# Kernel optimization log

Measured on AMD Instinct MI355X. Metric: run time of the kernel, lower is better.

## Reference

```python
import jax, jax.numpy as jnp
import numpy as np

B, S, D, H = 2, 2048, 512, 8
DK = D // H
MASK_VALUE = -1e9


def setup_inputs() -> dict:
    key = jax.random.key(0)
    ks = jax.random.split(key, 12)
    scale = 1.0 / np.sqrt(D)
    inp = {
        "query": jax.random.normal(ks[0], (B, S, D), jnp.float32),
        "key": jax.random.normal(ks[1], (B, S, D), jnp.float32),
        "value": jax.random.normal(ks[2], (B, S, D), jnp.float32),
        # causal mask, broadcastable over batch and heads
        "mask": jnp.tril(jnp.ones((S, S), jnp.int32))[None, None, :, :],
        "Wq": jax.random.normal(ks[3], (D, D), jnp.float32) * scale,
        "bq": jax.random.normal(ks[4], (D,), jnp.float32) * scale,
        "Wk": jax.random.normal(ks[5], (D, D), jnp.float32) * scale,
        "bk": jax.random.normal(ks[6], (D,), jnp.float32) * scale,
        "Wv": jax.random.normal(ks[7], (D, D), jnp.float32) * scale,
        "bv": jax.random.normal(ks[8], (D,), jnp.float32) * scale,
        "Wo": jax.random.normal(ks[9], (D, D), jnp.float32) * scale,
        "bo": jax.random.normal(ks[10], (D,), jnp.float32) * scale,
    }
    return inp


def reference(query, key, value, mask, Wq, bq, Wk, bk, Wv, bv, Wo, bo):
    # linear projections (torch Linear: x @ W.T + b)
    q = query @ Wq.T + bq
    k = key @ Wk.T + bk
    v = value @ Wv.T + bv
    # split heads: [B,S,D] -> [B,H,S,DK]
    q = q.reshape(B, S, H, DK).transpose(0, 2, 1, 3)
    k = k.reshape(B, S, H, DK).transpose(0, 2, 1, 3)
    v = v.reshape(B, S, H, DK).transpose(0, 2, 1, 3)
    # scaled dot-product attention with explicit [B,H,S,S] score matrix
    scores = jnp.einsum("bhqd,bhkd->bhqk", q, k) / jnp.sqrt(jnp.float32(DK))
    scores = jnp.where(mask == 0, jnp.float32(MASK_VALUE), scores)
    attn = jax.nn.softmax(scores, axis=-1)
    x = jnp.einsum("bhqk,bhkd->bhqd", attn, v)
    # merge heads: [B,H,S,DK] -> [B,S,D]
    x = x.transpose(0, 2, 1, 3).reshape(B, S, D)
    return x @ Wo.T + bo
```

## Files before the change

kernel.cpp:

```cpp
#include <hip/hip_runtime.h>
#include <hip/hip_bf16.h>

#define B_   2
#define S_   2048
#define D_   512
#define H_   8
#define DK_  64
#define M_   (B_*S_)

typedef float  floatx4 __attribute__((ext_vector_type(4)));
typedef __bf16 bf16x8  __attribute__((ext_vector_type(8)));

#define MFMA16x16x32(a,b,c) __builtin_amdgcn_mfma_f32_16x16x32_bf16((a),(b),(c),0,0,0)

static __device__ __forceinline__ void load_lds16(const void* g, void* l) {
  __builtin_amdgcn_global_load_lds(
      (const __attribute__((address_space(1))) void*)g,
      (__attribute__((address_space(3))) void*)l,
      16, 0, 0);
}

__global__ __launch_bounds__(256) void cvt_inputs(
    const float* __restrict__ w0, const float* __restrict__ w1,
    const float* __restrict__ w2, const float* __restrict__ w3,
    const float* __restrict__ x0, const float* __restrict__ x1,
    const float* __restrict__ x2,
    __bf16* __restrict__ out)
{
  const int idx = (blockIdx.x * 256 + threadIdx.x) * 4;
  const float* src;
  int off;
  if (idx < 1048576) {
    src = (idx < 524288) ? ((idx < 262144) ? w0 : w1)
                         : ((idx < 786432) ? w2 : w3);
    off = idx & 0x3FFFF;
  } else {
    const int i2 = idx - 1048576;
    const int xs = i2 >> 21;
    src = (xs == 0) ? x0 : (xs == 1) ? x1 : x2;
    off = i2 & 0x1FFFFF;
  }
  float4 v = *(const float4*)(src + off);
  __bf16* o = out + idx;
  o[0]=(__bf16)v.x; o[1]=(__bf16)v.y; o[2]=(__bf16)v.z; o[3]=(__bf16)v.w;
}


__global__ __launch_bounds__(256) void proj_qkv(
    const __bf16* __restrict__ Xb, const __bf16* __restrict__ Wball,
    const float* __restrict__ bq, const float* __restrict__ bk, const float* __restrict__ bv,
    __bf16* __restrict__ Qb, __bf16* __restrict__ Kb, __bf16* __restrict__ Vtb)
{
  __shared__ __align__(16) __bf16 abuf[2][128*32];
  __shared__ __align__(16) __bf16 bbuf[2][128*32];

  const int z = blockIdx.z;
  const __bf16* X    = Xb + (size_t)z * (M_*D_);
  const __bf16* W    = Wball + (size_t)z * (D_*D_);
  const float*  bias = (z==0) ? bq : (z==1) ? bk : bv;

  const int m0 = blockIdx.x * 128;
  const int n0 = blockIdx.y * 128;
  const int tid  = threadIdx.x;
  const int w    = tid >> 6;
  const int lane = tid & 63;
  const int lcol = lane & 15;
  const int quad = lane >> 4;
  const int wm = w >> 1, wn = w & 1;

  floatx4 zero = {0.f,0.f,0.f,0.f};
  floatx4 acc[4][4];
#pragma unroll
  for (int i = 0; i < 4; ++i)
#pragma unroll
    for (int nt = 0; nt < 4; ++nt) acc[i][nt] = zero;

  auto stage = [&](int bsel, int k0) {
#pragma unroll
    for (int j = 0; j < 2; ++j) {
      const int u0 = (j*4 + w) * 64;
      const int u  = u0 + lane;
      const int row = u >> 2, c16 = (u & 3) * 8;
      load_lds16(X + (size_t)(m0 + row)*D_ + k0 + c16,
                 (char*)&abuf[bsel][0] + u0*16);
      load_lds16(W + (size_t)(n0 + row)*D_ + k0 + c16,
                 (char*)&bbuf[bsel][0] + u0*16);
    }
  };

  stage(0, 0);
  for (int it = 0; it < 16; ++it) {
    __syncthreads();
    if (it + 1 < 16) stage((it+1)&1, (it+1)*32);
    const __bf16* ab = &abuf[it&1][0];
    const __bf16* bb = &bbuf[it&1][0];
    bf16x8 af[4], bf[4];
#pragma unroll
    for (int i = 0; i < 4; ++i)
      af[i] = *(const bf16x8*)(ab + (wm*64 + i*16 + lcol)*32 + quad*8);
#pragma unroll
    for (int nt = 0; nt < 4; ++nt)
      bf[nt] = *(const bf16x8*)(bb + (wn*64 + nt*16 + lcol)*32 + quad*8);
#pragma unroll
    for (int i = 0; i < 4; ++i)
#pragma unroll
      for (int nt = 0; nt < 4; ++nt)
        acc[i][nt] = MFMA16x16x32(af[i], bf[nt], acc[i][nt]);
  }

#pragma unroll
  for (int nt = 0; nt < 4; ++nt) {
    const int n = n0 + wn*64 + nt*16 + lcol;
    const float bias_n = bias[n];
    const int hh = n >> 6, dk = n & 63;
#pragma unroll
    for (int i = 0; i < 4; ++i)
#pragma unroll
      for (int r = 0; r < 4; ++r) {
        const int m  = m0 + wm*64 + i*16 + quad*4 + r;
        const int bb2 = m >> 11, ss = m & (S_-1);
        const float val = acc[i][nt][r] + bias_n;
        if (z == 0) {
          Qb[(((size_t)(bb2*H_+hh))*S_ + ss)*DK_ + dk] = (__bf16)val;
        } else if (z == 1) {
          const int cch = ss >> 6, klo = ss & 63;
          const int knt = klo >> 4, klc = klo & 15;
          const int ks = dk >> 5, qd = (dk >> 3) & 3, jj = dk & 7;
          Kb[((size_t)(bb2*H_+hh))*S_*DK_ + (size_t)cch*4096 +
             (((knt*2+ks)*64 + qd*16 + klc)*8 + jj)] = (__bf16)val;
        } else {
          const int cch = ss >> 6, klo = ss & 63;
          const int ks = klo >> 5, qd = (klo >> 3) & 3, jj = klo & 7;
          const int vnt = dk >> 4, vlc = dk & 15;
          Vtb[((size_t)(bb2*H_+hh))*DK_*S_ + (size_t)cch*4096 +
              (((vnt*2+ks)*64 + qd*16 + vlc)*8 + jj)] = (__bf16)val;
        }
      }
  }
}

__global__ __launch_bounds__(256) void attn_fwd(
    const __bf16* __restrict__ Qb, const __bf16* __restrict__ Kb,
    const __bf16* __restrict__ Vtb, __bf16* __restrict__ attnb)
{
  __shared__ __align__(16) __bf16 kbuf[2][64*64];
  __shared__ __align__(16) __bf16 vbuf[2][64*64];
  __shared__ __align__(16) __bf16 pbuf[4][16*72];

  const int tid  = threadIdx.x;
  const int w    = tid >> 6;
  const int lane = tid & 63;
  const int lcol = lane & 15;
  const int quad = lane >> 4;
  const int hh = blockIdx.y;
  const int bb = blockIdx.z;

  const int t   = 31 - blockIdx.x;
  const int q0  = t * 64;
  const int qr0 = q0 + w*16;

  const __bf16* Qp = Qb  + (size_t)(bb*H_ + hh) * S_ * DK_;
  const __bf16* Kp = Kb  + (size_t)(bb*H_ + hh) * S_ * DK_;
  const __bf16* Vp = Vtb + (size_t)(bb*H_ + hh) * DK_ * S_;

  const bf16x8 aq0 = *(const bf16x8*)(Qp + (size_t)(qr0 + lcol)*DK_ + quad*8);
  const bf16x8 aq1 = *(const bf16x8*)(Qp + (size_t)(qr0 + lcol)*DK_ + 32 + quad*8);

  floatx4 zero = {0.f,0.f,0.f,0.f};
  floatx4 acc[4] = {zero, zero, zero, zero};
  float lsum[4] = {0.f, 0.f, 0.f, 0.f};

  auto stage_chunk = [&](int bsel, int c) {
    const char* ksrc = (const char*)(Kp + (size_t)c * 4096);
    const char* vsrc = (const char*)(Vp + (size_t)c * 4096);
#pragma unroll
    for (int j = 0; j < 2; ++j) {
      const int off = w*2048 + j*1024;
      load_lds16(ksrc + off + lane*16, (char*)kbuf[bsel] + off);
      load_lds16(vsrc + off + lane*16, (char*)vbuf[bsel] + off);
    }
  };

  const int nch = t + 1;
  stage_chunk(0, 0);
  for (int c = 0; c < nch; ++c) {
    __syncthreads();
    if (c + 1 < nch) stage_chunk((c+1)&1, c+1);
    const int bsel = c & 1;
    const int k0 = c * 64;
    const __bf16* kb = kbuf[bsel];
    const __bf16* vb = vbuf[bsel];

    floatx4 s[4];
#pragma unroll
    for (int nt = 0; nt < 4; ++nt) {
      bf16x8 kf0 = *(const bf16x8*)(kb + (nt*2+0)*512 + lane*8);
      bf16x8 kf1 = *(const bf16x8*)(kb + (nt*2+1)*512 + lane*8);
      s[nt] = MFMA16x16x32(aq1, kf1, MFMA16x16x32(aq0, kf0, zero));
    }

    const bool edge = (k0 + 63 > qr0);
#pragma unroll
    for (int nt = 0; nt < 4; ++nt) {
#pragma unroll
      for (int r = 0; r < 4; ++r) {
        float p = __expf(s[nt][r] * 0.125f);
        if (edge) {
          const int qrow = qr0 + quad*4 + r;
          if (k0 + nt*16 + lcol > qrow) p = 0.f;
        }
        lsum[r] += p;
        pbuf[w][(quad*4 + r)*72 + nt*16 + lcol] = (__bf16)p;
      }
    }
    asm volatile("s_waitcnt lgkmcnt(0)" ::: "memory");

    const bf16x8 pa0 = *(const bf16x8*)(&pbuf[w][lcol*72 + quad*8]);
    const bf16x8 pa1 = *(const bf16x8*)(&pbuf[w][lcol*72 + 32 + quad*8]);
#pragma unroll
    for (int nt = 0; nt < 4; ++nt) {
      bf16x8 vf0 = *(const bf16x8*)(vb + (nt*2+0)*512 + lane*8);
      bf16x8 vf1 = *(const bf16x8*)(vb + (nt*2+1)*512 + lane*8);
      acc[nt] = MFMA16x16x32(pa0, vf0, acc[nt]);
      acc[nt] = MFMA16x16x32(pa1, vf1, acc[nt]);
    }
  }

  float rinv[4];
#pragma unroll
  for (int r = 0; r < 4; ++r) {
    float tv = lsum[r];
    tv += __shfl_xor(tv, 1, 16);
    tv += __shfl_xor(tv, 2, 16);
    tv += __shfl_xor(tv, 4, 16);
    tv += __shfl_xor(tv, 8, 16);
    rinv[r] = 1.0f / tv;
  }

#pragma unroll
  for (int nt = 0; nt < 4; ++nt)
#pragma unroll
    for (int r = 0; r < 4; ++r) {
      const int q = qr0 + quad*4 + r;
      attnb[((size_t)(bb*S_ + q)) * D_ + hh*DK_ + nt*16 + lcol] =
          (__bf16)(acc[nt][r] * rinv[r]);
    }
}

__global__ __launch_bounds__(256) void proj_out(
    const __bf16* __restrict__ attnb, const __bf16* __restrict__ Wob,
    const float* __restrict__ bo, float* __restrict__ out)
{
  __shared__ __align__(16) __bf16 abuf[2][128*32];
  __shared__ __align__(16) __bf16 bbuf[2][128*32];

  const int m0 = blockIdx.x * 128;
  const int n0 = blockIdx.y * 128;
  const int tid  = threadIdx.x;
  const int w    = tid >> 6;
  const int lane = tid & 63;
  const int lcol = lane & 15;
  const int quad = lane >> 4;
  const int wm = w >> 1, wn = w & 1;

  floatx4 zero = {0.f,0.f,0.f,0.f};
  floatx4 acc[4][4];
#pragma unroll
  for (int i = 0; i < 4; ++i)
#pragma unroll
    for (int nt = 0; nt < 4; ++nt) acc[i][nt] = zero;

  auto stage = [&](int bsel, int k0) {
#pragma unroll
    for (int j = 0; j < 2; ++j) {
      const int u0 = (j*4 + w) * 64;
      const int u  = u0 + lane;
      const int row = u >> 2, c16 = (u & 3) * 8;
      load_lds16(attnb + (size_t)(m0 + row)*D_ + k0 + c16,
                 (char*)&abuf[bsel][0] + u0*16);
      load_lds16(Wob + (size_t)(n0 + row)*D_ + k0 + c16,
                 (char*)&bbuf[bsel][0] + u0*16);
    }
  };

  stage(0, 0);
  for (int it = 0; it < 16; ++it) {
    __syncthreads();
    if (it + 1 < 16) stage((it+1)&1, (it+1)*32);
    const __bf16* ab = &abuf[it&1][0];
    const __bf16* bb = &bbuf[it&1][0];
    bf16x8 af[4], bf[4];
#pragma unroll
    for (int i = 0; i < 4; ++i)
      af[i] = *(const bf16x8*)(ab + (wm*64 + i*16 + lcol)*32 + quad*8);
#pragma unroll
    for (int nt = 0; nt < 4; ++nt)
      bf[nt] = *(const bf16x8*)(bb + (wn*64 + nt*16 + lcol)*32 + quad*8);
#pragma unroll
    for (int i = 0; i < 4; ++i)
#pragma unroll
      for (int nt = 0; nt < 4; ++nt)
        acc[i][nt] = MFMA16x16x32(af[i], bf[nt], acc[i][nt]);
  }

#pragma unroll
  for (int nt = 0; nt < 4; ++nt) {
    const int n = n0 + wn*64 + nt*16 + lcol;
    const float bias_n = bo[n];
#pragma unroll
    for (int i = 0; i < 4; ++i)
#pragma unroll
      for (int r = 0; r < 4; ++r) {
        const int m = m0 + wm*64 + i*16 + quad*4 + r;
        out[(size_t)m * D_ + n] = acc[i][nt][r] + bias_n;
      }
  }
}

extern "C" void kernel_launch(void* const* d_in, const int* in_sizes, int n_in,
                              void* d_out, int out_size, void* d_ws, size_t ws_size,
                              hipStream_t stream) {
  const float* q_in = (const float*)d_in[0];
  const float* k_in = (const float*)d_in[1];
  const float* v_in = (const float*)d_in[2];
  const float* Wq = (const float*)d_in[4];
  const float* bq = (const float*)d_in[5];
  const float* Wk = (const float*)d_in[6];
  const float* bk = (const float*)d_in[7];
  const float* Wv = (const float*)d_in[8];
  const float* bv = (const float*)d_in[9];
  const float* Wo = (const float*)d_in[10];
  const float* bo = (const float*)d_in[11];
  float* out = (float*)d_out;

  __bf16* ws    = (__bf16*)d_ws;
  __bf16* Qb    = ws;
  __bf16* Kb    = ws + 1*2097152;
  __bf16* Vtb   = ws + 2*2097152;
  __bf16* attnb = ws + 3*2097152;
  __bf16* Wb    = ws + 4*2097152;
  __bf16* Xb    = Wb + 4*262144;

  cvt_inputs<<<dim3(7168), dim3(256), 0, stream>>>(
      Wq, Wk, Wv, Wo, q_in, k_in, v_in, Wb);

  proj_qkv<<<dim3(M_/128, D_/128, 3), dim3(256), 0, stream>>>(
      Xb, Wb, bq, bk, bv, Qb, Kb, Vtb);

  attn_fwd<<<dim3(32, H_, B_), dim3(256), 0, stream>>>(Qb, Kb, Vtb, attnb);

  proj_out<<<dim3(M_/128, D_/128), dim3(256), 0, stream>>>(
      attnb, Wb + 3*262144, bo, out);
}
```

Measured before the change: 177.7 us.

## Stage QKV projection outputs through LDS and halve attention query tile

The QKV projection epilogue now writes its results into shared memory in the target per-head layouts (Q row-major, K and V pre-swizzled) and then copies them out with coalesced 16-byte stores, replacing scattered 2-byte global writes. The attention kernel moves from 64-row query tiles with 4 waves to 32-row tiles with 2 waves, doubling the grid to spread the causal workload across more blocks. In exchange, each attention block now reloads K/V chunks for fewer query rows, adding global and LDS traffic.

```diff
diff --git a/kernel.cpp b/kernel.cpp
--- a/kernel.cpp
+++ b/kernel.cpp
@@ -51,8 +51,7 @@
     const float* __restrict__ bq, const float* __restrict__ bk, const float* __restrict__ bv,
     __bf16* __restrict__ Qb, __bf16* __restrict__ Kb, __bf16* __restrict__ Vtb)
 {
-  __shared__ __align__(16) __bf16 abuf[2][128*32];
-  __shared__ __align__(16) __bf16 bbuf[2][128*32];
+  __shared__ __align__(16) __bf16 smem[16384];
 
   const int z = blockIdx.z;
   const __bf16* X    = Xb + (size_t)z * (M_*D_);
@@ -82,9 +81,9 @@
       const int u  = u0 + lane;
       const int row = u >> 2, c16 = (u & 3) * 8;
       load_lds16(X + (size_t)(m0 + row)*D_ + k0 + c16,
-                 (char*)&abuf[bsel][0] + u0*16);
+                 (char*)(smem + bsel*4096) + u0*16);
       load_lds16(W + (size_t)(n0 + row)*D_ + k0 + c16,
-                 (char*)&bbuf[bsel][0] + u0*16);
+                 (char*)(smem + 8192 + bsel*4096) + u0*16);
     }
   };
 
@@ -92,8 +91,8 @@
   for (int it = 0; it < 16; ++it) {
     __syncthreads();
     if (it + 1 < 16) stage((it+1)&1, (it+1)*32);
-    const __bf16* ab = &abuf[it&1][0];
-    const __bf16* bb = &bbuf[it&1][0];
+    const __bf16* ab = smem + (it&1)*4096;
+    const __bf16* bb = smem + 8192 + (it&1)*4096;
     bf16x8 af[4], bf[4];
 #pragma unroll
     for (int i = 0; i < 4; ++i)
@@ -108,44 +107,55 @@
         acc[i][nt] = MFMA16x16x32(af[i], bf[nt], acc[i][nt]);
   }
 
+  __syncthreads();
 #pragma unroll
   for (int nt = 0; nt < 4; ++nt) {
     const int n = n0 + wn*64 + nt*16 + lcol;
     const float bias_n = bias[n];
-    const int hh = n >> 6, dk = n & 63;
+    const int h_l = (n >> 6) & 1;
+    const int dk  = n & 63;
 #pragma unroll
     for (int i = 0; i < 4; ++i)
 #pragma unroll
       for (int r = 0; r < 4; ++r) {
-        const int m  = m0 + wm*64 + i*16 + quad*4 + r;
-        const int bb2 = m >> 11, ss = m & (S_-1);
+        const int m = m0 + wm*64 + i*16 + quad*4 + r;
         const float val = acc[i][nt][r] + bias_n;
+        const int p = h_l*2 + ((m >> 6) & 1);
+        const int klo = m & 63;
+        int off;
         if (z == 0) {
-          Qb[(((size_t)(bb2*H_+hh))*S_ + ss)*DK_ + dk] = (__bf16)val;
+          off = klo*64 + dk;
         } else if (z == 1) {
-          const int cch = ss >> 6, klo = ss & 63;
-          const int knt = klo >> 4, klc = klo & 15;
-          const int ks = dk >> 5, qd = (dk >> 3) & 3, jj = dk & 7;
-          Kb[((size_t)(bb2*H_+hh))*S_*DK_ + (size_t)cch*4096 +
-             (((knt*2+ks)*64 + qd*16 + klc)*8 + jj)] = (__bf16)val;
+          off = (((klo>>4)*2 + (dk>>5))*64 + ((dk>>3)&3)*16 + (klo&15))*8 + (dk&7);
         } else {
-          const int cch = ss >> 6, klo = ss & 63;
-          const int ks = klo >> 5, qd = (klo >> 3) & 3, jj = klo & 7;
-          const int vnt = dk >> 4, vlc = dk & 15;
-          Vtb[((size_t)(bb2*H_+hh))*DK_*S_ + (size_t)cch*4096 +
-              (((vnt*2+ks)*64 + qd*16 + vlc)*8 + jj)] = (__bf16)val;
+          off = (((dk>>4)*2 + (klo>>5))*64 + ((klo>>3)&3)*16 + (dk&15))*8 + (klo&7);
         }
+        smem[p*4096 + off] = (__bf16)val;
       }
   }
-}
-
-__global__ __launch_bounds__(256) void attn_fwd(
+  __syncthreads();
+
+  __bf16* dst = (z==0) ? Qb : (z==1) ? Kb : Vtb;
+  const int bb2  = m0 >> 11;
+  const int hh0  = n0 >> 6;
+  const int cc0  = (m0 & 2047) >> 6;
+#pragma unroll
+  for (int it2 = 0; it2 < 8; ++it2) {
+    const int u = it2*256 + tid;
+    const int p = u >> 9, o = u & 511;
+    const size_t base = ((size_t)(bb2*H_ + hh0 + (p>>1)))*(S_*DK_)
+                      + (size_t)(cc0 + (p&1))*4096;
+    *(bf16x8*)(dst + base + o*8) = *(const bf16x8*)(smem + p*4096 + o*8);
+  }
+}
+
+__global__ __launch_bounds__(128) void attn_fwd(
     const __bf16* __restrict__ Qb, const __bf16* __restrict__ Kb,
     const __bf16* __restrict__ Vtb, __bf16* __restrict__ attnb)
 {
-  __shared__ __align__(16) __bf16 kbuf[2][64*64];
-  __shared__ __align__(16) __bf16 vbuf[2][64*64];
-  __shared__ __align__(16) __bf16 pbuf[4][16*72];
+  __shared__ __align__(16) __bf16 kbuf[2][4096];
+  __shared__ __align__(16) __bf16 vbuf[2][4096];
+  __shared__ __align__(16) __bf16 pbuf[2][16*72];
 
   const int tid  = threadIdx.x;
   const int w    = tid >> 6;
@@ -155,8 +165,8 @@
   const int hh = blockIdx.y;
   const int bb = blockIdx.z;
 
-  const int t   = 31 - blockIdx.x;
-  const int q0  = t * 64;
+  const int t   = 63 - blockIdx.x;
+  const int q0  = t * 32;
   const int qr0 = q0 + w*16;
 
   const __bf16* Qp = Qb  + (size_t)(bb*H_ + hh) * S_ * DK_;
@@ -174,14 +184,14 @@
     const char* ksrc = (const char*)(Kp + (size_t)c * 4096);
     const char* vsrc = (const char*)(Vp + (size_t)c * 4096);
 #pragma unroll
-    for (int j = 0; j < 2; ++j) {
-      const int off = w*2048 + j*1024;
+    for (int j = 0; j < 4; ++j) {
+      const int off = (j*2 + w) * 1024;
       load_lds16(ksrc + off + lane*16, (char*)kbuf[bsel] + off);
       load_lds16(vsrc + off + lane*16, (char*)vbuf[bsel] + off);
     }
   };
 
-  const int nch = t + 1;
+  const int nch = (t + 2) >> 1;
   stage_chunk(0, 0);
   for (int c = 0; c < nch; ++c) {
     __syncthreads();
@@ -347,7 +357,7 @@
   proj_qkv<<<dim3(M_/128, D_/128, 3), dim3(256), 0, stream>>>(
       Xb, Wb, bq, bk, bv, Qb, Kb, Vtb);
 
-  attn_fwd<<<dim3(32, H_, B_), dim3(256), 0, stream>>>(Qb, Kb, Vtb, attnb);
+  attn_fwd<<<dim3(64, H_, B_), dim3(128), 0, stream>>>(Qb, Kb, Vtb, attnb);
 
   proj_out<<<dim3(M_/128, D_/128), dim3(256), 0, stream>>>(
       attnb, Wb + 3*262144, bo, out);
```

Measured after the change: 176.0 us. About the same (-0.9%).
